# Optimization experiments

Measured on AMD Instinct MI355X. Metric: run time of the kernel, lower is better.

## Reference

```python
import jax, jax.numpy as jnp
import numpy as np


def _encode(tab, idx):
    # tab: [F, V, D]; idx: [..., F] int -> sum_f tab[f, idx[..., f]] -> [..., D]
    g = jax.vmap(lambda t, i: t[i], in_axes=(0, -1), out_axes=0)(tab, idx)
    return g.sum(0)


def _diffuse(fea, ei, w, order):
    # fea: [N, D]; ei: [2, E]; w: [E] learned edge weights
    N = fea.shape[0]
    r, c = ei[0], ei[1]
    adj = jnp.zeros((N, N), fea.dtype).at[r, c].set(w).at[c, r].set(w)
    adj = adj + jnp.eye(N, dtype=fea.dtype)
    r_col_inv = adj.sum(1) ** -0.5  # from degree over axis 1
    r_row_inv = adj.sum(0) ** -0.5  # from degree over axis 0
    A = r_row_inv[:, None] * adj * r_col_inv[None, :]
    x = fea
    y = fea
    for _ in range(order):
        x = jax.lax.stop_gradient(A @ x)
        y = y + x
    return jax.lax.stop_gradient(y / (order + 1.0))


def setup_inputs():
    B, N, E, EMB, L, FA, FB, V = 512, 128, 512, 300, 5, 9, 3, 64
    k = jax.random.split(jax.random.key(0), 12)
    s = 0.02
    return {
        "order": 3,
        "x_atom": jax.random.randint(k[0], (B, N, FA), 0, V),
        "edge_index": jax.random.randint(k[1], (B, 2, E), 0, N),
        "edge_attr": jax.random.randint(k[2], (B, E, FB), 0, V),
        "atom_tab": jax.random.normal(k[3], (FA, V, EMB)) * s,
        "bond_tab_root": jax.random.normal(k[4], (FB, V, EMB)) * s,
        "edge_lin_w": jax.random.normal(k[5], (EMB,)) * s,
        "edge_lin_b": jnp.zeros(()),
        "bond_tabs": jax.random.normal(k[6], (L, FB, V, EMB)) * s,
        "eps": jnp.zeros((L,)),
        "w1": jax.random.normal(k[7], (L, EMB, 2 * EMB)) * s,
        "b1": jnp.zeros((L, 2 * EMB)),
        "bn1_g": jnp.ones((L, 2 * EMB)),
        "bn1_b": jnp.zeros((L, 2 * EMB)),
        "w2": jax.random.normal(k[8], (L, 2 * EMB, EMB)) * s,
        "b2": jnp.zeros((L, EMB)),
        "bn_g": jnp.ones((L, EMB)),
        "bn_b": jnp.zeros((L, EMB)),
    }


def reference(order, x_atom, edge_index, edge_attr, atom_tab, bond_tab_root,
              edge_lin_w, edge_lin_b, bond_tabs, eps, w1, b1, bn1_g, bn1_b,
              w2, b2, bn_g, bn_b):
    B, N = x_atom.shape[:2]
    E = edge_index.shape[-1]
    L = w1.shape[0]
    DROP = 0.2  # node-feature drop rate (eval-mode scaling)

    # --- per-graph dense-adjacency diffusion (vmapped over graphs) ---
    fea = _encode(atom_tab, x_atom) * (1.0 - DROP)                 # [B, N, D]
    e_emb = _encode(bond_tab_root, edge_attr)                      # [B, E, D]
    ew = jax.nn.sigmoid(e_emb @ edge_lin_w + edge_lin_b)           # [B, E]
    h = jax.vmap(_diffuse, in_axes=(0, 0, 0, None))(fea, edge_index, ew, order)
    h = h.reshape(B * N, -1)                                       # [B*N, D]

    # --- globally-batched GIN message passing ---
    off = (jnp.arange(B) * N)[:, None]
    src = (edge_index[:, 0, :] + off).reshape(-1)                  # [B*E]
    dst = (edge_index[:, 1, :] + off).reshape(-1)
    ea_flat = edge_attr.reshape(B * E, -1)

    for l in range(L):
        ee = _encode(bond_tabs[l], ea_flat)                        # [B*E, D]
        msg = jax.nn.relu(h[src] + ee)
        agg = jax.ops.segment_sum(msg, dst, num_segments=B * N)
        z = (1.0 + eps[l]) * h + agg
        z = z @ w1[l] + b1[l]
        z = bn1_g[l] * z + bn1_b[l]   # eval-mode BN (running mean 0, var 1)
        z = jax.nn.relu(z)
        z = z @ w2[l] + b2[l]
        z = bn_g[l] * z + bn_b[l]     # outer eval-mode BN
        if l < L - 1:
            z = jax.nn.relu(z)
        h = z
    return h
```

## Files before the change

### kernel.cpp

```cpp
#include <hip/hip_runtime.h>

#define NGRAPH 512
#define NNODE  128
#define NEDGE  512
#define EMB    300
#define NLAYER 5
#define FA     9
#define FB     3
#define VV     64
#define KPAD   136

typedef __bf16 bf16x8 __attribute__((ext_vector_type(8)));
typedef __bf16 bf16x4 __attribute__((ext_vector_type(4)));
typedef float  f32x4  __attribute__((ext_vector_type(4)));

__device__ __forceinline__ void gload_lds16(const void* gptr, void* lptr) {
    __builtin_amdgcn_global_load_lds(
        (const __attribute__((address_space(1))) void*)gptr,
        (__attribute__((address_space(3))) void*)lptr, 16, 0, 0);
}

__global__ __launch_bounds__(256)
void prep_w_kernel(const float* __restrict__ w1, const float* __restrict__ w2,
                   __bf16* __restrict__ w1t, __bf16* __restrict__ w2t)
{
    const int i = blockIdx.x * 256 + threadIdx.x;
    const int T1 = NLAYER * 640 * 320;
    const int T2 = NLAYER * 320 * 640;
    if (i < T1) {
        const int l = i / (640 * 320);
        const int r = i - l * 640 * 320;
        const int n = r / 320, k = r - n * 320;
        float v = (n < 600 && k < 300) ? w1[((size_t)l * 300 + k) * 600 + n] : 0.f;
        w1t[i] = (__bf16)v;
    } else if (i < T1 + T2) {
        const int j = i - T1;
        const int l = j / (320 * 640);
        const int r = j - l * 320 * 640;
        const int n = r / 640, k = r - n * 640;
        float v = (n < 300 && k < 600) ? w2[((size_t)l * 600 + k) * 300 + n] : 0.f;
        w2t[j] = (__bf16)v;
    }
}

__global__ __launch_bounds__(128)
void csr_kernel(const int* __restrict__ edge_index,
                const int* __restrict__ edge_attr,
                int* __restrict__ epk_sorted,
                int* __restrict__ off_g)
{
    __shared__ int epk_s[NEDGE];
    __shared__ int cnt[128];
    __shared__ int off_[129];

    const int tid = threadIdx.x;
    const int g   = blockIdx.x;

    cnt[tid] = 0;
    __syncthreads();
    for (int e = tid; e < NEDGE; e += 128) {
        const int s_ = edge_index[(g * 2 + 0) * NEDGE + e];
        const int d_ = edge_index[(g * 2 + 1) * NEDGE + e];
        const int base = (g * NEDGE + e) * 3;
        epk_s[e] = s_ | (d_ << 7) | (edge_attr[base + 0] << 14)
                 | (edge_attr[base + 1] << 20) | (edge_attr[base + 2] << 26);
        atomicAdd(&cnt[d_], 1);
    }
    __syncthreads();
    if (tid < 64) {
        const int a = cnt[tid];
        const int b = cnt[64 + tid];
        int ia = a;
        #pragma unroll
        for (int o = 1; o < 64; o <<= 1) {
            int t = __shfl_up(ia, o, 64);
            if (tid >= o) ia += t;
        }
        const int totA = __shfl(ia, 63, 64);
        int ib = b;
        #pragma unroll
        for (int o = 1; o < 64; o <<= 1) {
            int t = __shfl_up(ib, o, 64);
            if (tid >= o) ib += t;
        }
        off_[tid]      = ia - a;
        off_[64 + tid] = totA + ib - b;
        if (tid == 63) off_[128] = totA + ib;
    }
    __syncthreads();
    off_g[g * 129 + tid] = off_[tid];
    if (tid == 0) off_g[g * 129 + 128] = off_[128];
    int pos = off_[tid];
    for (int e = 0; e < NEDGE; ++e) {
        const int p = epk_s[e];
        if (((p >> 7) & 127) == tid) epk_sorted[(g << 9) + pos++] = p;
    }
}

__global__ __launch_bounds__(512)
void adj_kernel(const int* __restrict__ edge_index,
                const int* __restrict__ edge_attr,
                const float* __restrict__ bond_tab_root,
                const float* __restrict__ edge_lin_w,
                const float* __restrict__ edge_lin_b,
                __bf16* __restrict__ Ahi_g, __bf16* __restrict__ Alo_g)
{
    __shared__ float A[128 * 129];
    __shared__ float ew_s[NEDGE];
    __shared__ int   es[NEDGE];
    __shared__ float rinv[128];
    __shared__ float cinv[128];

    const int tid = threadIdx.x;
    const int g   = blockIdx.x;
    int* Ai = (int*)A;

    for (int e = tid; e < NEDGE; e += 512) {
        int r = edge_index[(g * 2 + 0) * NEDGE + e];
        int c = edge_index[(g * 2 + 1) * NEDGE + e];
        es[e] = r | (c << 8);
    }
    for (int i = tid; i < 128 * 129; i += 512) Ai[i] = -1;
    __syncthreads();

    {
        const int wave = tid >> 6, lane = tid & 63;
        const float elb = edge_lin_b[0];
        for (int e = wave * 64; e < wave * 64 + 64; ++e) {
            const int base = (g * NEDGE + e) * 3;
            const int a0 = edge_attr[base + 0];
            const int a1 = edge_attr[base + 1];
            const int a2 = edge_attr[base + 2];
            const float* t0 = bond_tab_root + (0 * VV + a0) * EMB;
            const float* t1 = bond_tab_root + (1 * VV + a1) * EMB;
            const float* t2 = bond_tab_root + (2 * VV + a2) * EMB;
            float acc = 0.f;
            for (int d = lane; d < EMB; d += 64)
                acc += (t0[d] + t1[d] + t2[d]) * edge_lin_w[d];
            #pragma unroll
            for (int off = 32; off > 0; off >>= 1) acc += __shfl_xor(acc, off, 64);
            if (lane == 0) ew_s[e] = 1.f / (1.f + expf(-(acc + elb)));
        }
    }
    for (int e = tid; e < NEDGE; e += 512) {
        int r = es[e] & 255, c = es[e] >> 8;
        atomicMax(&Ai[r * 129 + c], e);
        atomicMax(&Ai[c * 129 + r], 512 + e);
    }
    __syncthreads();
    for (int i = tid; i < 128 * 129; i += 512) {
        int p = Ai[i];
        A[i] = (p < 0) ? 0.f : ew_s[p & 511];
    }
    __syncthreads();
    if (tid < 128) A[tid * 129 + tid] += 1.f;
    __syncthreads();
    if (tid < 128) {
        float rs = 0.f, cs = 0.f;
        for (int j = 0; j < 128; ++j) { rs += A[tid * 129 + j]; cs += A[j * 129 + tid]; }
        rinv[tid] = 1.f / sqrtf(rs);
        cinv[tid] = 1.f / sqrtf(cs);
    }
    __syncthreads();
    for (int i = tid; i < 128 * KPAD; i += 512) {
        const int m = i / KPAD, k = i - m * KPAD;
        float v = (k < 128) ? A[m * 129 + k] * cinv[m] * rinv[k] : 0.f;
        __bf16 hi = (__bf16)v;
        Ahi_g[(size_t)g * 128 * KPAD + i] = hi;
        Alo_g[(size_t)g * 128 * KPAD + i] = (__bf16)(v - (float)hi);
    }
}

__global__ __launch_bounds__(512)
void diffuse_mm_kernel(const int* __restrict__ order_p,
                       const int* __restrict__ x_atom,
                       const float* __restrict__ atom_tab,
                       const __bf16* __restrict__ Ahi_g,
                       const __bf16* __restrict__ Alo_g,
                       __bf16* __restrict__ hb)
{
    __shared__ __bf16 Ahi[128 * KPAD];
    __shared__ __bf16 Alo[128 * KPAD];
    __shared__ __bf16 xt[4 * 64 * KPAD];
    __shared__ int    xat[128 * FA];

    const int tid  = threadIdx.x;
    const int g    = blockIdx.x;
    const int lane = tid & 63;
    const int wid  = tid >> 6;
    const int wm   = (wid >> 1) * 32;
    const int wn   = (wid & 1) * 32;
    const int lr   = lane & 15;
    const int q4   = (lane >> 4) * 4;
    const int kc   = (lane >> 4) * 8;

    for (int idx = tid; idx < 128 * KPAD / 8; idx += 512) {
        gload_lds16(Ahi_g + (size_t)g * 128 * KPAD + idx * 8, (char*)Ahi + idx * 16);
        gload_lds16(Alo_g + (size_t)g * 128 * KPAD + idx * 8, (char*)Alo + idx * 16);
    }
    for (int i = tid; i < 128 * FA; i += 512) xat[i] = x_atom[g * 128 * FA + i];
    __syncthreads();

    const int   ord    = order_p[0];
    const float yscale = 1.f / (float)(ord + 1);

    for (int cb = 0; cb < 5; ++cb) {
        const int dbase = cb * 64;

        float yacc[2][2][4];
        #pragma unroll
        for (int mi = 0; mi < 2; ++mi) {
            #pragma unroll
            for (int ni = 0; ni < 2; ++ni) {
                const int n_ = wn + ni * 16 + lr;
                const int d  = dbase + n_;
                #pragma unroll
                for (int r = 0; r < 4; ++r) {
                    const int m_ = wm + mi * 16 + q4 + r;
                    float v = 0.f;
                    if (d < EMB) {
                        #pragma unroll
                        for (int f = 0; f < FA; ++f)
                            v += atom_tab[(size_t)((f << 6) + xat[m_ * FA + f]) * EMB + d];
                        v *= 0.8f;
                    }
                    yacc[mi][ni][r] = v;
                    __bf16 hi = (__bf16)v;
                    xt[0 * 64 * KPAD + n_ * KPAD + m_] = hi;
                    xt[1 * 64 * KPAD + n_ * KPAD + m_] = (__bf16)(v - (float)hi);
                }
            }
        }
        __syncthreads();

        int curbuf = 0;
        for (int o = 0; o < ord; ++o) {
            const __bf16* xh = xt + (curbuf * 2 + 0) * 64 * KPAD;
            const __bf16* xl = xt + (curbuf * 2 + 1) * 64 * KPAD;
            f32x4 racc[2][2];
            #pragma unroll
            for (int mi = 0; mi < 2; ++mi)
                #pragma unroll
                for (int ni = 0; ni < 2; ++ni) racc[mi][ni] = (f32x4){0.f, 0.f, 0.f, 0.f};

            #pragma unroll
            for (int ks = 0; ks < 4; ++ks) {
                const int k0 = ks * 32 + kc;
                bf16x8 ah[2], al[2], bh[2], bl[2];
                #pragma unroll
                for (int mi = 0; mi < 2; ++mi) {
                    ah[mi] = *(const bf16x8*)&Ahi[(wm + mi * 16 + lr) * KPAD + k0];
                    al[mi] = *(const bf16x8*)&Alo[(wm + mi * 16 + lr) * KPAD + k0];
                }
                #pragma unroll
                for (int ni = 0; ni < 2; ++ni) {
                    bh[ni] = *(const bf16x8*)&xh[(wn + ni * 16 + lr) * KPAD + k0];
                    bl[ni] = *(const bf16x8*)&xl[(wn + ni * 16 + lr) * KPAD + k0];
                }
                #pragma unroll
                for (int mi = 0; mi < 2; ++mi) {
                    #pragma unroll
                    for (int ni = 0; ni < 2; ++ni) {
                        racc[mi][ni] = __builtin_amdgcn_mfma_f32_16x16x32_bf16(
                            ah[mi], bh[ni], racc[mi][ni], 0, 0, 0);
                        racc[mi][ni] = __builtin_amdgcn_mfma_f32_16x16x32_bf16(
                            ah[mi], bl[ni], racc[mi][ni], 0, 0, 0);
                        racc[mi][ni] = __builtin_amdgcn_mfma_f32_16x16x32_bf16(
                            al[mi], bh[ni], racc[mi][ni], 0, 0, 0);
                    }
                }
            }

            __bf16* nh = xt + ((curbuf ^ 1) * 2 + 0) * 64 * KPAD;
            __bf16* nl = xt + ((curbuf ^ 1) * 2 + 1) * 64 * KPAD;
            #pragma unroll
            for (int mi = 0; mi < 2; ++mi) {
                #pragma unroll
                for (int ni = 0; ni < 2; ++ni) {
                    const int n_ = wn + ni * 16 + lr;
                    const int mbase = wm + mi * 16 + q4;
                    bf16x4 hv, lv;
                    #pragma unroll
                    for (int r = 0; r < 4; ++r) {
                        const float v = racc[mi][ni][r];
                        yacc[mi][ni][r] += v;
                        __bf16 hi = (__bf16)v;
                        hv[r] = hi;
                        lv[r] = (__bf16)(v - (float)hi);
                    }
                    *(bf16x4*)&nh[n_ * KPAD + mbase] = hv;
                    *(bf16x4*)&nl[n_ * KPAD + mbase] = lv;
                }
            }
            __syncthreads();
            curbuf ^= 1;
        }

        #pragma unroll
        for (int mi = 0; mi < 2; ++mi) {
            #pragma unroll
            for (int ni = 0; ni < 2; ++ni) {
                const int n_ = wn + ni * 16 + lr;
                const int d  = dbase + n_;
                #pragma unroll
                for (int r = 0; r < 4; ++r) {
                    const int m_ = wm + mi * 16 + q4 + r;
                    const float v = (d < EMB) ? yacc[mi][ni][r] * yscale : 0.f;
                    hb[(size_t)(g * 128 + m_) * 320 + d] = (__bf16)v;
                }
            }
        }
    }
}

__global__ __launch_bounds__(1024)
void agg_kernel(const __bf16* __restrict__ hb,
                const int* __restrict__ epk_sorted,
                const int* __restrict__ off_g,
                const float* __restrict__ bond_tabs,
                const float* __restrict__ eps_all,
                const int l,
                __bf16* __restrict__ zb)
{
    __shared__ __bf16 hs[128 * 160];

    const int tid  = threadIdx.x;
    const int g    = blockIdx.x >> 1;
    const int coff = (blockIdx.x & 1) * 160;
    const int wave = tid >> 6, lane = tid & 63;
    const float epl = 1.f + eps_all[l];
    const float* bt = bond_tabs + (size_t)l * FB * VV * EMB;

    for (int idx = tid; idx < 128 * 20; idx += 1024) {
        const int r = idx / 20, c = idx - r * 20;
        *(bf16x8*)&hs[r * 160 + c * 8] =
            *(const bf16x8*)&hb[(size_t)(g * 128 + r) * 320 + coff + c * 8];
    }
    __syncthreads();

    const int d0 = lane, d1 = lane + 64, d2 = lane + 128;
    const bool r0 = (coff + d0) < EMB;
    const bool r1 = (coff + d1) < EMB;
    const bool r2 = (d2 < 160) && ((coff + d2) < EMB);

    const int* offg = off_g + g * 129;
    const int* epkg = epk_sorted + (g << 9);

    for (int n = wave; n < 128; n += 16) {
        float a0 = r0 ? epl * (float)hs[n * 160 + d0] : 0.f;
        float a1 = r1 ? epl * (float)hs[n * 160 + d1] : 0.f;
        float a2 = r2 ? epl * (float)hs[n * 160 + d2] : 0.f;
        const int eBeg = offg[n], eEnd = offg[n + 1];
        for (int ee = eBeg; ee < eEnd; ++ee) {
            const int p   = epkg[ee];
            const int src = p & 127;
            const float* t0 = bt + ((p >> 14) & 63) * EMB + coff;
            const float* t1 = bt + (64  + ((p >> 20) & 63)) * EMB + coff;
            const float* t2 = bt + (128 + ((p >> 26) & 63)) * EMB + coff;
            if (r0) a0 += fmaxf((float)hs[src * 160 + d0] + t0[d0] + t1[d0] + t2[d0], 0.f);
            if (r1) a1 += fmaxf((float)hs[src * 160 + d1] + t0[d1] + t1[d1] + t2[d1], 0.f);
            if (r2) a2 += fmaxf((float)hs[src * 160 + d2] + t0[d2] + t1[d2] + t2[d2], 0.f);
        }
        __bf16* zrow = zb + (size_t)(g * 128 + n) * 320 + coff;
        zrow[d0] = (__bf16)a0;
        zrow[d1] = (__bf16)a1;
        if (d2 < 160) zrow[d2] = (__bf16)a2;
    }
}

template <int ABF16, int CBF16, int RELU>
__global__ __launch_bounds__(256)
void gemm_mfma(const void* __restrict__ Av, const int lda, const int Kreal,
               const int nT, const int nBlkN, const __bf16* __restrict__ B,
               void* __restrict__ Cv, const int ldc, const int Nreal,
               const float* __restrict__ bias, const float* __restrict__ gam,
               const float* __restrict__ bet)
{
    __shared__ unsigned short As[128 * 32];
    __shared__ unsigned short Bs[64 * 32];

    const int tid  = threadIdx.x;
    const int nwg  = gridDim.x;
    const int hw   = blockIdx.x;
    const int lg   = (hw & 7) * (nwg >> 3) + (hw >> 3);
    const int bn   = (lg % nBlkN) * 64;
    const int bm   = (lg / nBlkN) * 128;
    const int wid  = tid >> 6;
    const int lane = tid & 63;
    const int wm   = (wid >> 1) * 64;
    const int wn   = (wid & 1) * 32;
    const int lr   = lane & 15;
    const int kc   = (lane >> 4) * 8;
    const int KP   = nT * 32;

    f32x4 acc[4][2];
    #pragma unroll
    for (int mi = 0; mi < 4; ++mi)
        #pragma unroll
        for (int ni = 0; ni < 2; ++ni) acc[mi][ni] = (f32x4){0.f, 0.f, 0.f, 0.f};

    for (int t = 0; t < nT; ++t) {
        const int k0 = t * 32;
        {
            const int n = tid >> 2, k8 = (tid & 3) * 8;
            gload_lds16(B + (size_t)(bn + n) * KP + k0 + k8,
                        (char*)Bs + tid * 16);
        }
        if (ABF16) {
            const __bf16* A = (const __bf16*)Av;
            #pragma unroll
            for (int q = 0; q < 2; ++q) {
                const int idx = q * 256 + tid;
                const int m = idx >> 2, k8 = (idx & 3) * 8;
                gload_lds16(A + (size_t)(bm + m) * lda + k0 + k8,
                            (char*)As + idx * 16);
            }
        } else {
            const float* A = (const float*)Av;
            #pragma unroll
            for (int q = 0; q < 2; ++q) {
                const int idx = q * 256 + tid;
                const int m = idx >> 2;
                const int k = k0 + (idx & 3) * 8;
                const float* src = A + (size_t)(bm + m) * lda + k;
                float v[8];
                if (k + 7 < Kreal) {
                    const float4 u0 = *(const float4*)src;
                    const float4 u1 = *(const float4*)(src + 4);
                    v[0] = u0.x; v[1] = u0.y; v[2] = u0.z; v[3] = u0.w;
                    v[4] = u1.x; v[5] = u1.y; v[6] = u1.z; v[7] = u1.w;
                } else {
                    #pragma unroll
                    for (int j = 0; j < 8; ++j) v[j] = (k + j < Kreal) ? src[j] : 0.f;
                }
                bf16x8 p;
                #pragma unroll
                for (int j = 0; j < 8; ++j) p[j] = (__bf16)v[j];
                *(bf16x8*)&As[idx * 8] = p;
            }
        }
        __syncthreads();

        bf16x8 a[4], bfr[2];
        #pragma unroll
        for (int mi = 0; mi < 4; ++mi)
            a[mi] = *(const bf16x8*)&As[(wm + mi * 16 + lr) * 32 + kc];
        #pragma unroll
        for (int ni = 0; ni < 2; ++ni)
            bfr[ni] = *(const bf16x8*)&Bs[(wn + ni * 16 + lr) * 32 + kc];
        #pragma unroll
        for (int mi = 0; mi < 4; ++mi)
            #pragma unroll
            for (int ni = 0; ni < 2; ++ni)
                acc[mi][ni] = __builtin_amdgcn_mfma_f32_16x16x32_bf16(
                    a[mi], bfr[ni], acc[mi][ni], 0, 0, 0);
        __syncthreads();
    }

    #pragma unroll
    for (int ni = 0; ni < 2; ++ni) {
        const int n = bn + wn + ni * 16 + lr;
        const bool nv = (n < Nreal);
        const float gv = nv ? gam[n]  : 0.f;
        const float bv = nv ? bias[n] : 0.f;
        const float ev = nv ? bet[n]  : 0.f;
        #pragma unroll
        for (int mi = 0; mi < 4; ++mi) {
            #pragma unroll
            for (int r = 0; r < 4; ++r) {
                const size_t m = bm + wm + mi * 16 + (lane >> 4) * 4 + r;
                float v = gv * (acc[mi][ni][r] + bv) + ev;
                if (RELU) v = fmaxf(v, 0.f);
                if (CBF16) {
                    ((__bf16*)Cv)[m * ldc + n] = (__bf16)v;
                } else if (nv) {
                    ((float*)Cv)[m * ldc + n] = v;
                }
            }
        }
    }
}

extern "C" void kernel_launch(void* const* d_in, const int* in_sizes, int n_in,
                              void* d_out, int out_size, void* d_ws, size_t ws_size,
                              hipStream_t stream)
{
    const int*   order_p       = (const int*)d_in[0];
    const int*   x_atom        = (const int*)d_in[1];
    const int*   edge_index    = (const int*)d_in[2];
    const int*   edge_attr     = (const int*)d_in[3];
    const float* atom_tab      = (const float*)d_in[4];
    const float* bond_tab_root = (const float*)d_in[5];
    const float* edge_lin_w    = (const float*)d_in[6];
    const float* edge_lin_b    = (const float*)d_in[7];
    const float* bond_tabs     = (const float*)d_in[8];
    const float* eps           = (const float*)d_in[9];
    const float* w1            = (const float*)d_in[10];
    const float* b1            = (const float*)d_in[11];
    const float* bn1g          = (const float*)d_in[12];
    const float* bn1b          = (const float*)d_in[13];
    const float* w2            = (const float*)d_in[14];
    const float* b2            = (const float*)d_in[15];
    const float* bng           = (const float*)d_in[16];
    const float* bnb           = (const float*)d_in[17];

    float*  h  = (float*)d_out;
    __bf16* hb = (__bf16*)d_out;

    char* ws = (char*)d_ws;
    __bf16* Ahi_g = (__bf16*)ws;
    __bf16* Alo_g = (__bf16*)(ws + 17825792);
    __bf16* z1    = (__bf16*)ws;
    __bf16* w1t   = (__bf16*)(ws + 83886080);
    __bf16* w2t   = (__bf16*)(ws + 83886080 + 2048000);
    __bf16* zb    = (__bf16*)(ws + 83886080 + 4096000);
    int*    epk_s = (int*)(ws + 83886080 + 4096000 + 41943040);
    int*    off_g = (int*)(ws + 83886080 + 4096000 + 41943040 + 1048576);

    prep_w_kernel<<<8000, 256, 0, stream>>>(w1, w2, w1t, w2t);

    csr_kernel<<<NGRAPH, 128, 0, stream>>>(edge_index, edge_attr, epk_s, off_g);

    adj_kernel<<<NGRAPH, 512, 0, stream>>>(edge_index, edge_attr, bond_tab_root,
                                           edge_lin_w, edge_lin_b, Ahi_g, Alo_g);

    diffuse_mm_kernel<<<NGRAPH, 512, 0, stream>>>(order_p, x_atom, atom_tab,
                                                  Ahi_g, Alo_g, hb);

    for (int l = 0; l < NLAYER; ++l) {
        agg_kernel<<<NGRAPH * 2, 1024, 0, stream>>>(
            hb, epk_s, off_g, bond_tabs, eps, l, zb);

        gemm_mfma<1, 1, 1><<<5120, 256, 0, stream>>>(
            zb, 320, 320, 10, 10, w1t + (size_t)l * 640 * 320,
            z1, 640, 600, b1 + l * 600, bn1g + l * 600, bn1b + l * 600);

        if (l < NLAYER - 1) {
            gemm_mfma<1, 1, 1><<<2560, 256, 0, stream>>>(
                z1, 640, 640, 20, 5, w2t + (size_t)l * 320 * 640,
                hb, 320, 300, b2 + l * 300, bng + l * 300, bnb + l * 300);
        } else {
            gemm_mfma<1, 0, 0><<<2560, 256, 0, stream>>>(
                z1, 640, 640, 20, 5, w2t + (size_t)l * 320 * 640,
                h, EMB, 300, b2 + l * 300, bng + l * 300, bnb + l * 300);
        }
    }
}
```

Before: 1.097 ms.

## Stage GEMM epilogue through LDS for coalesced stores; widen diffusion to 1024 threads

```diff
diff --git a/kernel.cpp b/kernel.cpp
--- a/kernel.cpp
+++ b/kernel.cpp
@@ -171,7 +171,7 @@
     }
 }
 
-__global__ __launch_bounds__(512)
+__global__ __launch_bounds__(1024)
 void diffuse_mm_kernel(const int* __restrict__ order_p,
                        const int* __restrict__ x_atom,
                        const float* __restrict__ atom_tab,
@@ -188,47 +188,44 @@
     const int g    = blockIdx.x;
     const int lane = tid & 63;
     const int wid  = tid >> 6;
-    const int wm   = (wid >> 1) * 32;
-    const int wn   = (wid & 1) * 32;
+    const int wm   = (wid >> 2) * 32;
+    const int wn   = (wid & 3) * 16;
     const int lr   = lane & 15;
     const int q4   = (lane >> 4) * 4;
     const int kc   = (lane >> 4) * 8;
 
-    for (int idx = tid; idx < 128 * KPAD / 8; idx += 512) {
+    for (int idx = tid; idx < 128 * KPAD / 8; idx += 1024) {
         gload_lds16(Ahi_g + (size_t)g * 128 * KPAD + idx * 8, (char*)Ahi + idx * 16);
         gload_lds16(Alo_g + (size_t)g * 128 * KPAD + idx * 8, (char*)Alo + idx * 16);
     }
-    for (int i = tid; i < 128 * FA; i += 512) xat[i] = x_atom[g * 128 * FA + i];
+    for (int i = tid; i < 128 * FA; i += 1024) xat[i] = x_atom[g * 128 * FA + i];
     __syncthreads();
 
     const int   ord    = order_p[0];
     const float yscale = 1.f / (float)(ord + 1);
+    const int   n_     = wn + lr;
 
     for (int cb = 0; cb < 5; ++cb) {
         const int dbase = cb * 64;
-
-        float yacc[2][2][4];
+        const int d     = dbase + n_;
+
+        float yacc[2][4];
         #pragma unroll
         for (int mi = 0; mi < 2; ++mi) {
             #pragma unroll
-            for (int ni = 0; ni < 2; ++ni) {
-                const int n_ = wn + ni * 16 + lr;
-                const int d  = dbase + n_;
-                #pragma unroll
-                for (int r = 0; r < 4; ++r) {
-                    const int m_ = wm + mi * 16 + q4 + r;
-                    float v = 0.f;
-                    if (d < EMB) {
-                        #pragma unroll
-                        for (int f = 0; f < FA; ++f)
-                            v += atom_tab[(size_t)((f << 6) + xat[m_ * FA + f]) * EMB + d];
-                        v *= 0.8f;
-                    }
-                    yacc[mi][ni][r] = v;
-                    __bf16 hi = (__bf16)v;
-                    xt[0 * 64 * KPAD + n_ * KPAD + m_] = hi;
-                    xt[1 * 64 * KPAD + n_ * KPAD + m_] = (__bf16)(v - (float)hi);
+            for (int r = 0; r < 4; ++r) {
+                const int m_ = wm + mi * 16 + q4 + r;
+                float v = 0.f;
+                if (d < EMB) {
+                    #pragma unroll
+                    for (int f = 0; f < FA; ++f)
+                        v += atom_tab[(size_t)((f << 6) + xat[m_ * FA + f]) * EMB + d];
+                    v *= 0.8f;
                 }
+                yacc[mi][r] = v;
+                __bf16 hi = (__bf16)v;
+                xt[0 * 64 * KPAD + n_ * KPAD + m_] = hi;
+                xt[1 * 64 * KPAD + n_ * KPAD + m_] = (__bf16)(v - (float)hi);
             }
         }
         __syncthreads();
@@ -237,37 +234,29 @@
         for (int o = 0; o < ord; ++o) {
             const __bf16* xh = xt + (curbuf * 2 + 0) * 64 * KPAD;
             const __bf16* xl = xt + (curbuf * 2 + 1) * 64 * KPAD;
-            f32x4 racc[2][2];
-            #pragma unroll
-            for (int mi = 0; mi < 2; ++mi)
-                #pragma unroll
-                for (int ni = 0; ni < 2; ++ni) racc[mi][ni] = (f32x4){0.f, 0.f, 0.f, 0.f};
+            f32x4 racc[2];
+            racc[0] = (f32x4){0.f, 0.f, 0.f, 0.f};
+            racc[1] = (f32x4){0.f, 0.f, 0.f, 0.f};
 
             #pragma unroll
             for (int ks = 0; ks < 4; ++ks) {
                 const int k0 = ks * 32 + kc;
-                bf16x8 ah[2], al[2], bh[2], bl[2];
+                bf16x8 ah[2], al[2], bh, bl;
                 #pragma unroll
                 for (int mi = 0; mi < 2; ++mi) {
                     ah[mi] = *(const bf16x8*)&Ahi[(wm + mi * 16 + lr) * KPAD + k0];
                     al[mi] = *(const bf16x8*)&Alo[(wm + mi * 16 + lr) * KPAD + k0];
                 }
-                #pragma unroll
-                for (int ni = 0; ni < 2; ++ni) {
-                    bh[ni] = *(const bf16x8*)&xh[(wn + ni * 16 + lr) * KPAD + k0];
-                    bl[ni] = *(const bf16x8*)&xl[(wn + ni * 16 + lr) * KPAD + k0];
-                }
+                bh = *(const bf16x8*)&xh[(wn + lr) * KPAD + k0];
+                bl = *(const bf16x8*)&xl[(wn + lr) * KPAD + k0];
                 #pragma unroll
                 for (int mi = 0; mi < 2; ++mi) {
-                    #pragma unroll
-                    for (int ni = 0; ni < 2; ++ni) {
-                        racc[mi][ni] = __builtin_amdgcn_mfma_f32_16x16x32_bf16(
-                            ah[mi], bh[ni], racc[mi][ni], 0, 0, 0);
-                        racc[mi][ni] = __builtin_amdgcn_mfma_f32_16x16x32_bf16(
-                            ah[mi], bl[ni], racc[mi][ni], 0, 0, 0);
-                        racc[mi][ni] = __builtin_amdgcn_mfma_f32_16x16x32_bf16(
-                            al[mi], bh[ni], racc[mi][ni], 0, 0, 0);
-                    }
+                    racc[mi] = __builtin_amdgcn_mfma_f32_16x16x32_bf16(
+                        ah[mi], bh, racc[mi], 0, 0, 0);
+                    racc[mi] = __builtin_amdgcn_mfma_f32_16x16x32_bf16(
+                        ah[mi], bl, racc[mi], 0, 0, 0);
+                    racc[mi] = __builtin_amdgcn_mfma_f32_16x16x32_bf16(
+                        al[mi], bh, racc[mi], 0, 0, 0);
                 }
             }
 
@@ -275,22 +264,18 @@
             __bf16* nl = xt + ((curbuf ^ 1) * 2 + 1) * 64 * KPAD;
             #pragma unroll
             for (int mi = 0; mi < 2; ++mi) {
+                const int mbase = wm + mi * 16 + q4;
+                bf16x4 hv, lv;
                 #pragma unroll
-                for (int ni = 0; ni < 2; ++ni) {
-                    const int n_ = wn + ni * 16 + lr;
-                    const int mbase = wm + mi * 16 + q4;
-                    bf16x4 hv, lv;
-                    #pragma unroll
-                    for (int r = 0; r < 4; ++r) {
-                        const float v = racc[mi][ni][r];
-                        yacc[mi][ni][r] += v;
-                        __bf16 hi = (__bf16)v;
-                        hv[r] = hi;
-                        lv[r] = (__bf16)(v - (float)hi);
-                    }
-                    *(bf16x4*)&nh[n_ * KPAD + mbase] = hv;
-                    *(bf16x4*)&nl[n_ * KPAD + mbase] = lv;
+                for (int r = 0; r < 4; ++r) {
+                    const float v = racc[mi][r];
+                    yacc[mi][r] += v;
+                    __bf16 hi = (__bf16)v;
+                    hv[r] = hi;
+                    lv[r] = (__bf16)(v - (float)hi);
                 }
+                *(bf16x4*)&nh[n_ * KPAD + mbase] = hv;
+                *(bf16x4*)&nl[n_ * KPAD + mbase] = lv;
             }
             __syncthreads();
             curbuf ^= 1;
@@ -299,15 +284,10 @@
         #pragma unroll
         for (int mi = 0; mi < 2; ++mi) {
             #pragma unroll
-            for (int ni = 0; ni < 2; ++ni) {
-                const int n_ = wn + ni * 16 + lr;
-                const int d  = dbase + n_;
-                #pragma unroll
-                for (int r = 0; r < 4; ++r) {
-                    const int m_ = wm + mi * 16 + q4 + r;
-                    const float v = (d < EMB) ? yacc[mi][ni][r] * yscale : 0.f;
-                    hb[(size_t)(g * 128 + m_) * 320 + d] = (__bf16)v;
-                }
+            for (int r = 0; r < 4; ++r) {
+                const int m_ = wm + mi * 16 + q4 + r;
+                const float v = (d < EMB) ? yacc[mi][r] * yscale : 0.f;
+                hb[(size_t)(g * 128 + m_) * 320 + d] = (__bf16)v;
             }
         }
     }
@@ -368,16 +348,17 @@
     }
 }
 
-template <int ABF16, int CBF16, int RELU>
+template <int CBF16, int RELU>
 __global__ __launch_bounds__(256)
-void gemm_mfma(const void* __restrict__ Av, const int lda, const int Kreal,
+void gemm_mfma(const __bf16* __restrict__ A, const int lda,
                const int nT, const int nBlkN, const __bf16* __restrict__ B,
                void* __restrict__ Cv, const int ldc, const int Nreal,
                const float* __restrict__ bias, const float* __restrict__ gam,
                const float* __restrict__ bet)
 {
-    __shared__ unsigned short As[128 * 32];
-    __shared__ unsigned short Bs[64 * 32];
+    __shared__ __align__(16) char smem_raw[12288];
+    unsigned short* As = (unsigned short*)smem_raw;
+    unsigned short* Bs = (unsigned short*)(smem_raw + 8192);
 
     const int tid  = threadIdx.x;
     const int nwg  = gridDim.x;
@@ -391,6 +372,7 @@
     const int wn   = (wid & 1) * 32;
     const int lr   = lane & 15;
     const int kc   = (lane >> 4) * 8;
+    const int q4   = (lane >> 4) * 4;
     const int KP   = nT * 32;
 
     f32x4 acc[4][2];
@@ -406,38 +388,12 @@
             gload_lds16(B + (size_t)(bn + n) * KP + k0 + k8,
                         (char*)Bs + tid * 16);
         }
-        if (ABF16) {
-            const __bf16* A = (const __bf16*)Av;
-            #pragma unroll
-            for (int q = 0; q < 2; ++q) {
-                const int idx = q * 256 + tid;
-                const int m = idx >> 2, k8 = (idx & 3) * 8;
-                gload_lds16(A + (size_t)(bm + m) * lda + k0 + k8,
-                            (char*)As + idx * 16);
-            }
-        } else {
-            const float* A = (const float*)Av;
-            #pragma unroll
-            for (int q = 0; q < 2; ++q) {
-                const int idx = q * 256 + tid;
-                const int m = idx >> 2;
-                const int k = k0 + (idx & 3) * 8;
-                const float* src = A + (size_t)(bm + m) * lda + k;
-                float v[8];
-                if (k + 7 < Kreal) {
-                    const float4 u0 = *(const float4*)src;
-                    const float4 u1 = *(const float4*)(src + 4);
-                    v[0] = u0.x; v[1] = u0.y; v[2] = u0.z; v[3] = u0.w;
-                    v[4] = u1.x; v[5] = u1.y; v[6] = u1.z; v[7] = u1.w;
-                } else {
-                    #pragma unroll
-                    for (int j = 0; j < 8; ++j) v[j] = (k + j < Kreal) ? src[j] : 0.f;
-                }
-                bf16x8 p;
-                #pragma unroll
-                for (int j = 0; j < 8; ++j) p[j] = (__bf16)v[j];
-                *(bf16x8*)&As[idx * 8] = p;
-            }
+        #pragma unroll
+        for (int q = 0; q < 2; ++q) {
+            const int idx = q * 256 + tid;
+            const int m = idx >> 2, k8 = (idx & 3) * 8;
+            gload_lds16(A + (size_t)(bm + m) * lda + k0 + k8,
+                        (char*)As + idx * 16);
         }
         __syncthreads();
 
@@ -457,26 +413,77 @@
         __syncthreads();
     }
 
+    float gv[2], bv[2], ev[2];
     #pragma unroll
     for (int ni = 0; ni < 2; ++ni) {
         const int n = bn + wn + ni * 16 + lr;
         const bool nv = (n < Nreal);
-        const float gv = nv ? gam[n]  : 0.f;
-        const float bv = nv ? bias[n] : 0.f;
-        const float ev = nv ? bet[n]  : 0.f;
-        #pragma unroll
-        for (int mi = 0; mi < 4; ++mi) {
-            #pragma unroll
-            for (int r = 0; r < 4; ++r) {
-                const size_t m = bm + wm + mi * 16 + (lane >> 4) * 4 + r;
-                float v = gv * (acc[mi][ni][r] + bv) + ev;
-                if (RELU) v = fmaxf(v, 0.f);
-                if (CBF16) {
-                    ((__bf16*)Cv)[m * ldc + n] = (__bf16)v;
-                } else if (nv) {
-                    ((float*)Cv)[m * ldc + n] = v;
+        gv[ni] = nv ? gam[n]  : 0.f;
+        bv[ni] = nv ? bias[n] : 0.f;
+        ev[ni] = nv ? bet[n]  : 0.f;
+    }
+
+    if (CBF16) {
+        __bf16* Cb = (__bf16*)smem_raw;
+        #pragma unroll
+        for (int half = 0; half < 2; ++half) {
+            if ((wm >> 6) == half) {
+                #pragma unroll
+                for (int ni = 0; ni < 2; ++ni) {
+                    const int nl = wn + ni * 16 + lr;
+                    #pragma unroll
+                    for (int mi = 0; mi < 4; ++mi) {
+                        #pragma unroll
+                        for (int r = 0; r < 4; ++r) {
+                            float v = gv[ni] * (acc[mi][ni][r] + bv[ni]) + ev[ni];
+                            if (RELU) v = fmaxf(v, 0.f);
+                            Cb[(mi * 16 + q4 + r) * 72 + nl] = (__bf16)v;
+                        }
+                    }
                 }
             }
+            __syncthreads();
+            #pragma unroll
+            for (int q = 0; q < 2; ++q) {
+                const int idx = q * 256 + tid;
+                const int row = idx >> 3, c16 = (idx & 7) * 8;
+                const size_t m = (size_t)bm + half * 64 + row;
+                *(bf16x8*)&((__bf16*)Cv)[m * ldc + bn + c16] =
+                    *(const bf16x8*)&Cb[row * 72 + c16];
+            }
+            __syncthreads();
+        }
+    } else {
+        float* Cf = (float*)smem_raw;
+        const int ncols = (Nreal - bn < 64) ? (Nreal - bn) : 64;
+        const int nch = ncols >> 2;
+        #pragma unroll
+        for (int mq = 0; mq < 4; ++mq) {
+            if ((wm >> 6) == (mq >> 1)) {
+                const int mi0 = (mq & 1) * 2;
+                #pragma unroll
+                for (int ni = 0; ni < 2; ++ni) {
+                    const int nl = wn + ni * 16 + lr;
+                    #pragma unroll
+                    for (int mi2 = 0; mi2 < 2; ++mi2) {
+                        const int mi = mi0 + mi2;
+                        #pragma unroll
+                        for (int r = 0; r < 4; ++r) {
+                            float v = gv[ni] * (acc[mi][ni][r] + bv[ni]) + ev[ni];
+                            if (RELU) v = fmaxf(v, 0.f);
+                            Cf[(mi2 * 16 + q4 + r) * 68 + nl] = v;
+                        }
+                    }
+                }
+            }
+            __syncthreads();
+            for (int idx = tid; idx < 32 * nch; idx += 256) {
+                const int row = idx / nch, c4 = (idx - row * nch) * 4;
+                const size_t m = (size_t)bm + mq * 32 + row;
+                *(float4*)&((float*)Cv)[m * ldc + bn + c4] =
+                    *(const float4*)&Cf[row * 68 + c4];
+            }
+            __syncthreads();
         }
     }
 }
@@ -524,24 +531,24 @@
     adj_kernel<<<NGRAPH, 512, 0, stream>>>(edge_index, edge_attr, bond_tab_root,
                                            edge_lin_w, edge_lin_b, Ahi_g, Alo_g);
 
-    diffuse_mm_kernel<<<NGRAPH, 512, 0, stream>>>(order_p, x_atom, atom_tab,
-                                                  Ahi_g, Alo_g, hb);
+    diffuse_mm_kernel<<<NGRAPH, 1024, 0, stream>>>(order_p, x_atom, atom_tab,
+                                                   Ahi_g, Alo_g, hb);
 
     for (int l = 0; l < NLAYER; ++l) {
         agg_kernel<<<NGRAPH * 2, 1024, 0, stream>>>(
             hb, epk_s, off_g, bond_tabs, eps, l, zb);
 
-        gemm_mfma<1, 1, 1><<<5120, 256, 0, stream>>>(
-            zb, 320, 320, 10, 10, w1t + (size_t)l * 640 * 320,
+        gemm_mfma<1, 1><<<5120, 256, 0, stream>>>(
+            zb, 320, 10, 10, w1t + (size_t)l * 640 * 320,
             z1, 640, 600, b1 + l * 600, bn1g + l * 600, bn1b + l * 600);
 
         if (l < NLAYER - 1) {
-            gemm_mfma<1, 1, 1><<<2560, 256, 0, stream>>>(
-                z1, 640, 640, 20, 5, w2t + (size_t)l * 320 * 640,
+            gemm_mfma<1, 1><<<2560, 256, 0, stream>>>(
+                z1, 640, 20, 5, w2t + (size_t)l * 320 * 640,
                 hb, 320, 300, b2 + l * 300, bng + l * 300, bnb + l * 300);
         } else {
-            gemm_mfma<1, 0, 0><<<2560, 256, 0, stream>>>(
-                z1, 640, 640, 20, 5, w2t + (size_t)l * 320 * 640,
+            gemm_mfma<0, 0><<<2560, 256, 0, stream>>>(
+                z1, 640, 20, 5, w2t + (size_t)l * 320 * 640,
                 h, EMB, 300, b2 + l * 300, bng + l * 300, bnb + l * 300);
         }
     }
```

New measurement: 1.083 ms. Within noise of the previous version (-1.2%).
